# Performance work log

Hardware: AMD Instinct MI355X
Metric: run time of the kernel (lower is better)

Reference implementation:

```python
import jax, jax.numpy as jnp
import numpy as np

N, E, DIM, STEPS, POSD = 50000, 800000, 128, 4, 3
LN_EPS = 1e-5


def setup_inputs() -> dict:
    key = jax.random.key(0)
    ks = jax.random.split(key, 12)
    x = jax.random.normal(ks[0], (N, DIM), dtype=jnp.float32)
    pos = jax.random.normal(ks[1], (N, POSD), dtype=jnp.float32)
    edge_index = jax.random.randint(ks[2], (2, E), 0, N, dtype=jnp.int64)
    s_msg = 1.0 / np.sqrt(2 * DIM + POSD)
    s_upd = 1.0 / np.sqrt(2 * DIM)
    msg_W = jax.random.uniform(ks[3], (STEPS, 2 * DIM + POSD, DIM), jnp.float32, -s_msg, s_msg)
    msg_b = jax.random.uniform(ks[4], (STEPS, DIM), jnp.float32, -s_msg, s_msg)
    msg_g = jnp.ones((STEPS, DIM), jnp.float32)
    msg_be = jnp.zeros((STEPS, DIM), jnp.float32)
    upd_W = jax.random.uniform(ks[5], (STEPS, 2 * DIM, DIM), jnp.float32, -s_upd, s_upd)
    upd_b = jax.random.uniform(ks[6], (STEPS, DIM), jnp.float32, -s_upd, s_upd)
    upd_g = jnp.ones((STEPS, DIM), jnp.float32)
    upd_be = jnp.zeros((STEPS, DIM), jnp.float32)
    return dict(x=x, pos=pos, edge_index=edge_index, msg_W=msg_W, msg_b=msg_b,
                msg_g=msg_g, msg_be=msg_be, upd_W=upd_W, upd_b=upd_b,
                upd_g=upd_g, upd_be=upd_be)


def _layernorm(x, g, b):
    mu = jnp.mean(x, axis=-1, keepdims=True)
    var = jnp.mean(jnp.square(x - mu), axis=-1, keepdims=True)
    return (x - mu) * jax.lax.rsqrt(var + LN_EPS) * g + b


def _mpnn_forward(x, pos, edge_index, msg_W, msg_b, msg_g, msg_be, upd_W, upd_b, upd_g, upd_be):
    row, col = edge_index[0], edge_index[1]
    edge_attr = pos[row] - pos[col]  # [E, 3]
    n_nodes = x.shape[0]
    # receiver counts (constant across steps)
    counts = jax.ops.segment_sum(jnp.ones((edge_index.shape[1],), x.dtype), col, num_segments=n_nodes)
    denom = jnp.maximum(counts, 1.0)[:, None]  # clamp(min=1)
    h = x
    for s in range(msg_W.shape[0]):
        # message: MLP([h_row, h_col, edge_attr]) with GELU + LayerNorm
        m_in = jnp.concatenate([h[row], h[col], edge_attr], axis=-1)  # [E, 2D+3]
        m = jnp.dot(m_in, msg_W[s]) + msg_b[s]
        m = _layernorm(jax.nn.gelu(m, approximate=False), msg_g[s], msg_be[s])
        # aggregate: scatter_mean over receivers (col)
        agg = jax.ops.segment_sum(m, col, num_segments=n_nodes) / denom  # [N, D]
        # update: MLP([h, agg]) with LayerNorm, residual
        u_in = jnp.concatenate([h, agg], axis=-1)  # [N, 2D]
        u = _layernorm(jnp.dot(u_in, upd_W[s]) + upd_b[s], upd_g[s], upd_be[s])
        h = h + u
    return h


def reference(x, pos, edge_index, msg_W, msg_b, msg_g, msg_be, upd_W, upd_b, upd_g, upd_be):
    return _mpnn_forward(x, pos, edge_index, msg_W, msg_b, msg_g, msg_be, upd_W, upd_b, upd_g, upd_be)
```

## Files before the change

kernel.cpp:

```cpp
#include <hip/hip_runtime.h>
#include <math.h>

#define NN   50000
#define NE   800000
#define DIM  128
#define KMSG 259
#define KUPD 256
#define STEPS 4
#define LN_EPS 1e-5f

#define EPB 64
#define NKSU 8
#define NKSP 4
#define NNT  8
#define NNTP 16
#define UPITCH 264
#define NBLK ((NN + 255) / 256)

typedef __attribute__((ext_vector_type(8))) short bf16x8;
typedef __attribute__((ext_vector_type(4))) float f32x4;
typedef unsigned short u16;

__device__ __forceinline__ u16 f2b(float f) {
    union { float f; unsigned u; } v; v.f = f;
    unsigned r = (v.u + 0x7fffu + ((v.u >> 16) & 1u)) >> 16;
    return (u16)r;
}

__device__ __forceinline__ float b2f(u16 v) {
    union { unsigned u; float f; } t; t.u = ((unsigned)v) << 16; return t.f;
}

__device__ __forceinline__ float gelu_fast(float x) {
    float y = 0.7978845608f * (x + 0.044715f * x * x * x);
    float s = __expf(-2.0f * y);
    return x * __builtin_amdgcn_rcpf(1.0f + s);
}

__global__ void count_kernel(const int* __restrict__ ei, int* __restrict__ cnt) {
    int e = blockIdx.x * 256 + threadIdx.x;
    if (e < NE) atomicAdd(&cnt[ei[NE + e]], 1);
}

__global__ void dinv_kernel(const int* __restrict__ cnt, float* __restrict__ dinv) {
    int n = blockIdx.x * 256 + threadIdx.x;
    if (n < NN) dinv[n] = 1.0f / fmaxf((float)cnt[n], 1.0f);
}

__global__ void scanA_kernel(const int* __restrict__ cnt, int* __restrict__ bsum) {
    int n = blockIdx.x * 256 + threadIdx.x;
    int c = (n < NN) ? cnt[n] : 0;
    #pragma unroll
    for (int off = 1; off < 64; off <<= 1) c += __shfl_xor(c, off);
    __shared__ int ws[4];
    if ((threadIdx.x & 63) == 0) ws[threadIdx.x >> 6] = c;
    __syncthreads();
    if (threadIdx.x == 0) bsum[blockIdx.x] = ws[0] + ws[1] + ws[2] + ws[3];
}

__global__ void scanB_kernel(const int* __restrict__ bsum, int* __restrict__ boff) {
    __shared__ int sh[256];
    int tid = threadIdx.x;
    int v = (tid < NBLK) ? bsum[tid] : 0;
    sh[tid] = v;
    __syncthreads();
    for (int off = 1; off < 256; off <<= 1) {
        int t = (tid >= off) ? sh[tid - off] : 0;
        __syncthreads();
        sh[tid] += t;
        __syncthreads();
    }
    if (tid < NBLK) boff[tid] = sh[tid] - v;
}

__global__ void scanC_kernel(const int* __restrict__ cnt, const int* __restrict__ boff,
                             int* __restrict__ cursor, int* __restrict__ csr0) {
    __shared__ int sh[256];
    int tid = threadIdx.x;
    int n = blockIdx.x * 256 + tid;
    int c = (n < NN) ? cnt[n] : 0;
    sh[tid] = c;
    __syncthreads();
    for (int off = 1; off < 256; off <<= 1) {
        int t = (tid >= off) ? sh[tid - off] : 0;
        __syncthreads();
        sh[tid] += t;
        __syncthreads();
    }
    int ex = sh[tid] - c + boff[blockIdx.x];
    if (n < NN) { cursor[n] = ex; csr0[n] = ex; }
}

__global__ void scatter_kernel(const int* __restrict__ ei, int* __restrict__ cursor,
                               int* __restrict__ rowS) {
    int e = blockIdx.x * 256 + threadIdx.x;
    if (e < NE) {
        int c = ei[NE + e];
        int p = atomicAdd(&cursor[c], 1);
        rowS[p] = ei[e];
    }
}

__global__ void h2b_kernel(const float* __restrict__ h, u16* __restrict__ hb) {
    int i = blockIdx.x * 256 + threadIdx.x;
    if (i < NN * DIM / 4) {
        float4 v = ((const float4*)h)[i];
        ushort4 o;
        o.x = f2b(v.x); o.y = f2b(v.y); o.z = f2b(v.z); o.w = f2b(v.w);
        ((ushort4*)hb)[i] = o;
    }
}

__global__ void posw_kernel(const float* __restrict__ pos, float* __restrict__ posW) {
    int n = blockIdx.x * 256 + threadIdx.x;
    if (n < NN) {
        float4 o = {pos[n*3+0], pos[n*3+1], pos[n*3+2], 0.f};
        ((float4*)posW)[n] = o;
    }
}

__global__ void wupd_kernel(const float* __restrict__ W, u16* __restrict__ Wf) {
    int i = blockIdx.x * 256 + threadIdx.x;
    if (i >= STEPS * NKSU * NNT * 64 * 8) return;
    int j    = i & 7;
    int lane = (i >> 3) & 63;
    int nt   = (i >> 9) & 7;
    int ks   = (i >> 12) & 7;
    int s    = i >> 15;
    int k = ks * 32 + (lane >> 4) * 8 + j;
    int n = nt * 16 + (lane & 15);
    Wf[i] = f2b(W[((size_t)s * KUPD + k) * DIM + n]);
}

__global__ void wpre_kernel(const float* __restrict__ W, u16* __restrict__ Wf) {
    int i = blockIdx.x * 256 + threadIdx.x;
    if (i >= STEPS * NKSP * NNTP * 64 * 8) return;
    int j    = i & 7;
    int lane = (i >> 3) & 63;
    int nt   = (i >> 9) & 15;
    int ks   = (i >> 13) & 3;
    int s    = (i >> 15) & 3;
    int k = ks * 32 + (lane >> 4) * 8 + j;
    int n = nt * 16 + (lane & 15);
    int krow = (n < 128) ? k : 128 + k;
    int ncol = n & 127;
    Wf[i] = f2b(W[((size_t)s * KMSG + krow) * DIM + ncol]);
}

__global__ __launch_bounds__(256, 4)
void pre_kernel(const u16* __restrict__ hb, const u16* __restrict__ Wf,
                u16* __restrict__ XW1b, float* __restrict__ XW2) {
    __shared__ u16 Au[64][136];

    const int tid = threadIdx.x;
    const int nbase = blockIdx.x * 64;

    for (int i = tid; i < 1024; i += 256) {
        int e = i >> 4, c = i & 15, d = c * 8;
        int node = nbase + e;
        bf16x8 v = (node < NN) ? *(const bf16x8*)(hb + (size_t)node * DIM + d)
                               : (bf16x8){0,0,0,0,0,0,0,0};
        *(bf16x8*)&Au[e][d] = v;
    }
    __syncthreads();

    const int wave = tid >> 6;
    const int lane = tid & 63;
    const int l15 = lane & 15;
    const int lhi = lane >> 4;

    f32x4 acc[NNTP];
    #pragma unroll
    for (int t = 0; t < NNTP; ++t) acc[t] = (f32x4){0.f, 0.f, 0.f, 0.f};

    const u16* Arow = &Au[wave * 16 + l15][lhi * 8];

    #pragma unroll
    for (int ks = 0; ks < NKSP; ++ks) {
        bf16x8 a = *(const bf16x8*)(Arow + ks * 32);
        const u16* wp = Wf + (size_t)(ks * NNTP) * 512 + lane * 8;
        #pragma unroll
        for (int nt = 0; nt < NNTP; ++nt) {
            bf16x8 b = *(const bf16x8*)(wp + nt * 512);
            acc[nt] = __builtin_amdgcn_mfma_f32_16x16x32_bf16(a, b, acc[nt], 0, 0, 0);
        }
    }

    #pragma unroll
    for (int r = 0; r < 4; ++r) {
        int node = nbase + wave * 16 + lhi * 4 + r;
        if (node < NN) {
            u16*   o1 = XW1b + (size_t)node * DIM + l15;
            float* o2 = XW2  + (size_t)node * DIM + l15;
            #pragma unroll
            for (int t = 0; t < 8; ++t)  o1[t * 16] = f2b(acc[t][r]);
            #pragma unroll
            for (int t = 8; t < 16; ++t) o2[(t - 8) * 16] = acc[t][r];
        }
    }
}

__global__ __launch_bounds__(256, 4)
void edge_kernel(const u16* __restrict__ XW1b, const float* __restrict__ XW2,
                 const float* __restrict__ posW,
                 const int* __restrict__ rowS, const int* __restrict__ csr0,
                 const int* __restrict__ cnt,
                 const float* __restrict__ Wstep, const float* __restrict__ bias,
                 const float* __restrict__ gam, const float* __restrict__ bet,
                 float* __restrict__ agg) {
    const int tid = threadIdx.x;
    const int sub = tid & 31;
    const int n = (blockIdx.x * 256 + tid) >> 5;
    if (n >= NN) return;

    const int e0 = csr0[n];
    const int e1 = e0 + cnt[n];

    float4 bi = ((const float4*)bias)[sub];
    float4 gm = ((const float4*)gam)[sub];
    float4 bt = ((const float4*)bet)[sub];
    const float* W3 = Wstep + (size_t)256 * DIM;
    float4 w3a = ((const float4*)(W3))[sub];
    float4 w3b = ((const float4*)(W3 + DIM))[sub];
    float4 w3c = ((const float4*)(W3 + 2 * DIM))[sub];

    const float4*  XW24 = (const float4*)XW2;
    const ushort4* XW14 = (const ushort4*)XW1b;
    const float4*  P4   = (const float4*)posW;

    float4 x2 = XW24[(size_t)n * 32 + sub];
    float4 pc = P4[n];
    float4 base;
    base.x = x2.x + bi.x; base.y = x2.y + bi.y;
    base.z = x2.z + bi.z; base.w = x2.w + bi.w;

    float4 racc = {0.f, 0.f, 0.f, 0.f};

    if (e0 < e1) {
        int row = rowS[e0];
        ushort4 x1u = XW14[(size_t)row * 32 + sub];
        float4 pr = P4[row];

        for (int e = e0; e < e1; ++e) {
            int nrow = 0; ushort4 nx1u = x1u; float4 npr = pr;
            if (e + 1 < e1) {
                nrow = rowS[e+1];
                nx1u = XW14[(size_t)nrow * 32 + sub];
                npr = P4[nrow];
            }

            float ea0 = pr.x - pc.x, ea1 = pr.y - pc.y, ea2 = pr.z - pc.z;
            float4 m;
            m.x = b2f(x1u.x) + base.x + ea0*w3a.x + ea1*w3b.x + ea2*w3c.x;
            m.y = b2f(x1u.y) + base.y + ea0*w3a.y + ea1*w3b.y + ea2*w3c.y;
            m.z = b2f(x1u.z) + base.z + ea0*w3a.z + ea1*w3b.z + ea2*w3c.z;
            m.w = b2f(x1u.w) + base.w + ea0*w3a.w + ea1*w3b.w + ea2*w3c.w;
            m.x = gelu_fast(m.x); m.y = gelu_fast(m.y);
            m.z = gelu_fast(m.z); m.w = gelu_fast(m.w);

            float s = m.x + m.y + m.z + m.w;
            float q = m.x*m.x + m.y*m.y + m.z*m.z + m.w*m.w;
            #pragma unroll
            for (int off = 1; off < 32; off <<= 1) {
                s += __shfl_xor(s, off);
                q += __shfl_xor(q, off);
            }
            float mu  = s * (1.0f / 128.0f);
            float var = q * (1.0f / 128.0f) - mu * mu;
            float rs  = rsqrtf(var + LN_EPS);

            racc.x += (m.x - mu) * rs * gm.x + bt.x;
            racc.y += (m.y - mu) * rs * gm.y + bt.y;
            racc.z += (m.z - mu) * rs * gm.z + bt.z;
            racc.w += (m.w - mu) * rs * gm.w + bt.w;

            row = nrow; x1u = nx1u; pr = npr;
        }
    }

    *(float4*)(agg + (size_t)n * DIM + sub * 4) = racc;
}

__global__ __launch_bounds__(256, 4)
void upd_kernel(float* __restrict__ h, u16* __restrict__ hb,
                const float* __restrict__ agg, const float* __restrict__ dinv,
                const u16* __restrict__ Wf, const float* __restrict__ bias,
                const float* __restrict__ gam, const float* __restrict__ bet) {
    __shared__ u16 Au[EPB][UPITCH];

    const int tid = threadIdx.x;
    const int nbase = blockIdx.x * EPB;

    for (int i = tid; i < 1024; i += 256) {
        int e = i >> 4, c = i & 15, d = c * 8;
        int node = nbase + e;
        bf16x8 v = (node < NN) ? *(const bf16x8*)(hb + (size_t)node * DIM + d)
                               : (bf16x8){0,0,0,0,0,0,0,0};
        *(bf16x8*)&Au[e][d] = v;
    }
    for (int i = tid; i < 2048; i += 256) {
        int e = i >> 5, c = i & 31, d = c * 4;
        int node = nbase + e;
        u16 o0 = 0, o1 = 0, o2 = 0, o3 = 0;
        if (node < NN) {
            float dv = dinv[node];
            float4 a = ((const float4*)agg)[(size_t)node * 32 + c];
            o0 = f2b(a.x * dv); o1 = f2b(a.y * dv);
            o2 = f2b(a.z * dv); o3 = f2b(a.w * dv);
        }
        ushort4 o = {o0, o1, o2, o3};
        *(ushort4*)&Au[e][DIM + d] = o;
    }
    __syncthreads();

    const int wave = tid >> 6;
    const int lane = tid & 63;
    const int l15 = lane & 15;
    const int lhi = lane >> 4;

    f32x4 acc[NNT];
    #pragma unroll
    for (int t = 0; t < NNT; ++t) acc[t] = (f32x4){0.f, 0.f, 0.f, 0.f};

    const u16* Arow = &Au[wave * 16 + l15][lhi * 8];

    #pragma unroll
    for (int ks = 0; ks < NKSU; ++ks) {
        bf16x8 a = *(const bf16x8*)(Arow + ks * 32);
        const u16* wp = Wf + (size_t)(ks * NNT) * 512 + lane * 8;
        #pragma unroll
        for (int nt = 0; nt < NNT; ++nt) {
            bf16x8 b = *(const bf16x8*)(wp + nt * 512);
            acc[nt] = __builtin_amdgcn_mfma_f32_16x16x32_bf16(a, b, acc[nt], 0, 0, 0);
        }
    }

    float bs[NNT], gs[NNT], be[NNT];
    #pragma unroll
    for (int t = 0; t < NNT; ++t) {
        int n = t * 16 + l15;
        bs[t] = bias[n]; gs[t] = gam[n]; be[t] = bet[n];
    }

    float s0[4] = {0.f, 0.f, 0.f, 0.f}, q0[4] = {0.f, 0.f, 0.f, 0.f};
    #pragma unroll
    for (int t = 0; t < NNT; ++t)
        #pragma unroll
        for (int r = 0; r < 4; ++r) {
            float x = acc[t][r] + bs[t];
            acc[t][r] = x;
            s0[r] += x; q0[r] += x * x;
        }
    #pragma unroll
    for (int r = 0; r < 4; ++r)
        #pragma unroll
        for (int off = 1; off < 16; off <<= 1) {
            s0[r] += __shfl_xor(s0[r], off);
            q0[r] += __shfl_xor(q0[r], off);
        }

    #pragma unroll
    for (int r = 0; r < 4; ++r) {
        int node = nbase + wave * 16 + lhi * 4 + r;
        if (node >= NN) continue;
        float mu  = s0[r] * (1.0f / 128.0f);
        float var = q0[r] * (1.0f / 128.0f) - mu * mu;
        float rs  = rsqrtf(var + LN_EPS);
        #pragma unroll
        for (int t = 0; t < NNT; ++t) {
            int n = t * 16 + l15;
            float u = (acc[t][r] - mu) * rs * gs[t] + be[t];
            size_t idx = (size_t)node * DIM + n;
            float out = h[idx] + u;
            h[idx] = out;
            hb[idx] = f2b(out);
        }
    }
}

extern "C" void kernel_launch(void* const* d_in, const int* in_sizes, int n_in,
                              void* d_out, int out_size, void* d_ws, size_t ws_size,
                              hipStream_t stream) {
    const float* x      = (const float*)d_in[0];
    const float* pos    = (const float*)d_in[1];
    const int*   ei     = (const int*)d_in[2];
    const float* msg_W  = (const float*)d_in[3];
    const float* msg_b  = (const float*)d_in[4];
    const float* msg_g  = (const float*)d_in[5];
    const float* msg_be = (const float*)d_in[6];
    const float* upd_W  = (const float*)d_in[7];
    const float* upd_b  = (const float*)d_in[8];
    const float* upd_g  = (const float*)d_in[9];
    const float* upd_be = (const float*)d_in[10];

    float* h = (float*)d_out;
    char*  ws = (char*)d_ws;
    float* agg    = (float*)ws;
    float* dinv   = (float*)(ws + 25600000);
    u16*   hb     = (u16*)(ws + 25800192);
    u16*   Wfu    = (u16*)(ws + 38600192);
    u16*   Wfp    = (u16*)(ws + 38862336);
    int*   cnt    = (int*)(ws + 39124480);
    int*   cursor = (int*)(ws + 39324672);
    int*   csr0   = (int*)(ws + 39524864);
    int*   rowS   = (int*)(ws + 39724864);
    int*   bsum   = (int*)(ws + 42924864);
    int*   boff   = (int*)(ws + 42925888);
    float* XW2    = (float*)(ws + 45924864);
    u16*   XW1b   = (u16*)(ws + 71524864);
    float* posW   = (float*)(ws + 84324864);

    hipMemcpyAsync(h, x, (size_t)NN * DIM * sizeof(float),
                   hipMemcpyDeviceToDevice, stream);
    h2b_kernel<<<(NN * DIM / 4 + 255) / 256, 256, 0, stream>>>(x, hb);
    posw_kernel<<<(NN + 255) / 256, 256, 0, stream>>>(pos, posW);

    hipMemsetAsync(cnt, 0, (size_t)NN * sizeof(int), stream);
    count_kernel<<<(NE + 255) / 256, 256, 0, stream>>>(ei, cnt);
    scanA_kernel<<<NBLK, 256, 0, stream>>>(cnt, bsum);
    scanB_kernel<<<1, 256, 0, stream>>>(bsum, boff);
    scanC_kernel<<<NBLK, 256, 0, stream>>>(cnt, boff, cursor, csr0);
    scatter_kernel<<<(NE + 255) / 256, 256, 0, stream>>>(ei, cursor, rowS);
    dinv_kernel<<<(NN + 255) / 256, 256, 0, stream>>>(cnt, dinv);

    wupd_kernel<<<(STEPS * NKSU * NNT * 64 * 8 + 255) / 256, 256, 0, stream>>>(upd_W, Wfu);
    wpre_kernel<<<(STEPS * NKSP * NNTP * 64 * 8 + 255) / 256, 256, 0, stream>>>(msg_W, Wfp);

    const int EBLOCKS = (NN * 32 + 255) / 256;

    for (int s = 0; s < STEPS; ++s) {
        pre_kernel<<<(NN + 63) / 64, 256, 0, stream>>>(
            hb, Wfp + (size_t)s * NKSP * NNTP * 512, XW1b, XW2);
        edge_kernel<<<EBLOCKS, 256, 0, stream>>>(
            XW1b, XW2, posW, rowS, csr0, cnt, msg_W + (size_t)s * KMSG * DIM,
            msg_b + (size_t)s * DIM, msg_g + (size_t)s * DIM,
            msg_be + (size_t)s * DIM, agg);
        upd_kernel<<<(NN + EPB - 1) / EPB, 256, 0, stream>>>(
            h, hb, agg, dinv, Wfu + (size_t)s * NKSU * NNT * 512,
            upd_b + (size_t)s * DIM, upd_g + (size_t)s * DIM,
            upd_be + (size_t)s * DIM);
    }
}
```

Baseline: 800.2 us.

## Hoist LayerNorm affine out of edge loop, unroll edges, emit bf16 mean aggregate

```diff
diff --git a/kernel.cpp b/kernel.cpp
--- a/kernel.cpp
+++ b/kernel.cpp
@@ -204,17 +204,24 @@
 void edge_kernel(const u16* __restrict__ XW1b, const float* __restrict__ XW2,
                  const float* __restrict__ posW,
                  const int* __restrict__ rowS, const int* __restrict__ csr0,
-                 const int* __restrict__ cnt,
+                 const int* __restrict__ cnt, const float* __restrict__ dinv,
                  const float* __restrict__ Wstep, const float* __restrict__ bias,
                  const float* __restrict__ gam, const float* __restrict__ bet,
-                 float* __restrict__ agg) {
+                 u16* __restrict__ aggb) {
     const int tid = threadIdx.x;
     const int sub = tid & 31;
     const int n = (blockIdx.x * 256 + tid) >> 5;
     if (n >= NN) return;
 
+    u16* out = aggb + (size_t)n * DIM + sub * 4;
+    const int deg = cnt[n];
+    if (deg == 0) {
+        ushort4 z = {0, 0, 0, 0};
+        *(ushort4*)out = z;
+        return;
+    }
     const int e0 = csr0[n];
-    const int e1 = e0 + cnt[n];
+    const int e1 = e0 + deg;
 
     float4 bi = ((const float4*)bias)[sub];
     float4 gm = ((const float4*)gam)[sub];
@@ -234,56 +241,77 @@
     base.x = x2.x + bi.x; base.y = x2.y + bi.y;
     base.z = x2.z + bi.z; base.w = x2.w + bi.w;
 
-    float4 racc = {0.f, 0.f, 0.f, 0.f};
-
-    if (e0 < e1) {
-        int row = rowS[e0];
-        ushort4 x1u = XW14[(size_t)row * 32 + sub];
-        float4 pr = P4[row];
-
-        for (int e = e0; e < e1; ++e) {
-            int nrow = 0; ushort4 nx1u = x1u; float4 npr = pr;
-            if (e + 1 < e1) {
-                nrow = rowS[e+1];
-                nx1u = XW14[(size_t)nrow * 32 + sub];
-                npr = P4[nrow];
+    float4 R1 = {0.f, 0.f, 0.f, 0.f};
+    float  S  = 0.f;
+
+    auto edge_body = [&](ushort4 x1u, float4 pr) {
+        float ea0 = pr.x - pc.x, ea1 = pr.y - pc.y, ea2 = pr.z - pc.z;
+        float4 m;
+        m.x = b2f(x1u.x) + base.x + ea0*w3a.x + ea1*w3b.x + ea2*w3c.x;
+        m.y = b2f(x1u.y) + base.y + ea0*w3a.y + ea1*w3b.y + ea2*w3c.y;
+        m.z = b2f(x1u.z) + base.z + ea0*w3a.z + ea1*w3b.z + ea2*w3c.z;
+        m.w = b2f(x1u.w) + base.w + ea0*w3a.w + ea1*w3b.w + ea2*w3c.w;
+        m.x = gelu_fast(m.x); m.y = gelu_fast(m.y);
+        m.z = gelu_fast(m.z); m.w = gelu_fast(m.w);
+
+        float s = m.x + m.y + m.z + m.w;
+        float q = m.x*m.x + m.y*m.y + m.z*m.z + m.w*m.w;
+        #pragma unroll
+        for (int off = 1; off < 32; off <<= 1) {
+            s += __shfl_xor(s, off);
+            q += __shfl_xor(q, off);
+        }
+        float mu  = s * (1.0f / 128.0f);
+        float var = q * (1.0f / 128.0f) - mu * mu;
+        float rs  = rsqrtf(var + LN_EPS);
+
+        R1.x = fmaf(m.x, rs, R1.x);
+        R1.y = fmaf(m.y, rs, R1.y);
+        R1.z = fmaf(m.z, rs, R1.z);
+        R1.w = fmaf(m.w, rs, R1.w);
+        S = fmaf(mu, rs, S);
+    };
+
+    int e = e0;
+    if (deg & 1) {
+        int r = rowS[e];
+        edge_body(XW14[(size_t)r * 32 + sub], P4[r]);
+        ++e;
+    }
+    if (e < e1) {
+        int rA = rowS[e], rB = rowS[e + 1];
+        ushort4 xA = XW14[(size_t)rA * 32 + sub];
+        ushort4 xB = XW14[(size_t)rB * 32 + sub];
+        float4 prA = P4[rA], prB = P4[rB];
+        while (e < e1) {
+            ushort4 xC = xA, xD = xB;
+            float4 prC = prA, prD = prB;
+            if (e + 3 < e1) {
+                int rC = rowS[e + 2], rD = rowS[e + 3];
+                xC = XW14[(size_t)rC * 32 + sub];
+                xD = XW14[(size_t)rD * 32 + sub];
+                prC = P4[rC]; prD = P4[rD];
             }
-
-            float ea0 = pr.x - pc.x, ea1 = pr.y - pc.y, ea2 = pr.z - pc.z;
-            float4 m;
-            m.x = b2f(x1u.x) + base.x + ea0*w3a.x + ea1*w3b.x + ea2*w3c.x;
-            m.y = b2f(x1u.y) + base.y + ea0*w3a.y + ea1*w3b.y + ea2*w3c.y;
-            m.z = b2f(x1u.z) + base.z + ea0*w3a.z + ea1*w3b.z + ea2*w3c.z;
-            m.w = b2f(x1u.w) + base.w + ea0*w3a.w + ea1*w3b.w + ea2*w3c.w;
-            m.x = gelu_fast(m.x); m.y = gelu_fast(m.y);
-            m.z = gelu_fast(m.z); m.w = gelu_fast(m.w);
-
-            float s = m.x + m.y + m.z + m.w;
-            float q = m.x*m.x + m.y*m.y + m.z*m.z + m.w*m.w;
-            #pragma unroll
-            for (int off = 1; off < 32; off <<= 1) {
-                s += __shfl_xor(s, off);
-                q += __shfl_xor(q, off);
-            }
-            float mu  = s * (1.0f / 128.0f);
-            float var = q * (1.0f / 128.0f) - mu * mu;
-            float rs  = rsqrtf(var + LN_EPS);
-
-            racc.x += (m.x - mu) * rs * gm.x + bt.x;
-            racc.y += (m.y - mu) * rs * gm.y + bt.y;
-            racc.z += (m.z - mu) * rs * gm.z + bt.z;
-            racc.w += (m.w - mu) * rs * gm.w + bt.w;
-
-            row = nrow; x1u = nx1u; pr = npr;
-        }
-    }
-
-    *(float4*)(agg + (size_t)n * DIM + sub * 4) = racc;
+            edge_body(xA, prA);
+            edge_body(xB, prB);
+            e += 2;
+            xA = xC; xB = xD; prA = prC; prB = prD;
+        }
+    }
+
+    float dv = dinv[n];
+    float4 o;
+    o.x = fmaf(gm.x * (R1.x - S), dv, bt.x);
+    o.y = fmaf(gm.y * (R1.y - S), dv, bt.y);
+    o.z = fmaf(gm.z * (R1.z - S), dv, bt.z);
+    o.w = fmaf(gm.w * (R1.w - S), dv, bt.w);
+    ushort4 ob = {f2b(o.x), f2b(o.y), f2b(o.z), f2b(o.w)};
+    *(ushort4*)out = ob;
 }
 
 __global__ __launch_bounds__(256, 4)
 void upd_kernel(float* __restrict__ h, u16* __restrict__ hb,
-                const float* __restrict__ agg, const float* __restrict__ dinv,
+                const u16* __restrict__ aggb,
                 const u16* __restrict__ Wf, const float* __restrict__ bias,
                 const float* __restrict__ gam, const float* __restrict__ bet) {
     __shared__ u16 Au[EPB][UPITCH];
@@ -298,18 +326,12 @@
                                : (bf16x8){0,0,0,0,0,0,0,0};
         *(bf16x8*)&Au[e][d] = v;
     }
-    for (int i = tid; i < 2048; i += 256) {
-        int e = i >> 5, c = i & 31, d = c * 4;
+    for (int i = tid; i < 1024; i += 256) {
+        int e = i >> 4, c = i & 15, d = c * 8;
         int node = nbase + e;
-        u16 o0 = 0, o1 = 0, o2 = 0, o3 = 0;
-        if (node < NN) {
-            float dv = dinv[node];
-            float4 a = ((const float4*)agg)[(size_t)node * 32 + c];
-            o0 = f2b(a.x * dv); o1 = f2b(a.y * dv);
-            o2 = f2b(a.z * dv); o3 = f2b(a.w * dv);
-        }
-        ushort4 o = {o0, o1, o2, o3};
-        *(ushort4*)&Au[e][DIM + d] = o;
+        bf16x8 v = (node < NN) ? *(const bf16x8*)(aggb + (size_t)node * DIM + d)
+                               : (bf16x8){0,0,0,0,0,0,0,0};
+        *(bf16x8*)&Au[e][DIM + d] = v;
     }
     __syncthreads();
 
@@ -395,7 +417,7 @@
 
     float* h = (float*)d_out;
     char*  ws = (char*)d_ws;
-    float* agg    = (float*)ws;
+    u16*   aggb   = (u16*)ws;
     float* dinv   = (float*)(ws + 25600000);
     u16*   hb     = (u16*)(ws + 25800192);
     u16*   Wfu    = (u16*)(ws + 38600192);
@@ -432,11 +454,12 @@
         pre_kernel<<<(NN + 63) / 64, 256, 0, stream>>>(
             hb, Wfp + (size_t)s * NKSP * NNTP * 512, XW1b, XW2);
         edge_kernel<<<EBLOCKS, 256, 0, stream>>>(
-            XW1b, XW2, posW, rowS, csr0, cnt, msg_W + (size_t)s * KMSG * DIM,
+            XW1b, XW2, posW, rowS, csr0, cnt, dinv,
+            msg_W + (size_t)s * KMSG * DIM,
             msg_b + (size_t)s * DIM, msg_g + (size_t)s * DIM,
-            msg_be + (size_t)s * DIM, agg);
+            msg_be + (size_t)s * DIM, aggb);
         upd_kernel<<<(NN + EPB - 1) / EPB, 256, 0, stream>>>(
-            h, hb, agg, dinv, Wfu + (size_t)s * NKSU * NNT * 512,
+            h, hb, aggb, Wfu + (size_t)s * NKSU * NNT * 512,
             upd_b + (size_t)s * DIM, upd_g + (size_t)s * DIM,
             upd_be + (size_t)s * DIM);
     }
```

Result: faster. 731.5 us (-8.6%).
